# Kernel optimization log

Hardware: AMD Instinct MI355X
Metric: run time of the kernel (lower is better)

Reference implementation:

```python
import jax, jax.numpy as jnp
import numpy as np

B, N, I, H, O, E, HD = 4, 2048, 32, 64, 32, 2, 2  # batch, nodes, in_dim, hidden, out, edgetypes, heads
D1 = H * HD * E  # layer-1 filter input dim (concat of all heads/edgetypes from layer 0)


def setup_inputs() -> dict:
    key = jax.random.key(0)
    ks = jax.random.split(key, 20)
    s = 0.1
    return {
        "nodes": jax.random.normal(ks[0], (B, N, I), jnp.float32),
        "edges": jax.random.normal(ks[1], (B, N, N, E), jnp.float32),
        "W_emb": jax.random.normal(ks[2], (I, H), jnp.float32) * s,
        "b_emb": jnp.zeros((H,), jnp.float32),
        "Wf0": jax.random.normal(ks[3], (E, HD, H, H), jnp.float32) * s,
        "w1_0": jax.random.normal(ks[4], (E, HD, H), jnp.float32) * s,
        "b1_0": jnp.zeros((E, HD), jnp.float32),
        "w2_0": jax.random.normal(ks[5], (E, HD, H), jnp.float32) * s,
        "b2_0": jnp.zeros((E, HD), jnp.float32),
        "bias0": jax.random.normal(ks[6], (HD, H), jnp.float32) * s,  # state_bias aliased across edgetypes (list-mult bug)
        "Wf1": jax.random.normal(ks[7], (E, HD, D1, H), jnp.float32) * s,
        "w1_1": jax.random.normal(ks[8], (E, HD, H), jnp.float32) * s,
        "b1_1": jnp.zeros((E, HD), jnp.float32),
        "w2_1": jax.random.normal(ks[9], (E, HD, H), jnp.float32) * s,
        "b2_1": jnp.zeros((E, HD), jnp.float32),
        "bias1": jax.random.normal(ks[10], (HD, H), jnp.float32) * s,
        "W_out": jax.random.normal(ks[11], (H, O), jnp.float32) * s,
        "b_out": jnp.zeros((O,), jnp.float32),
    }


def _gat_layer(state, Wf, w1, b1, w2, b2, bias, edges_t, last):
    # state: (B,N,Din); Wf: (E,HD,Din,H); edges_t: (E,B,N,N)
    Wh = jnp.einsum('bnd,ehdk->ehbnk', state, Wf)                     # (E,HD,B,N,H)
    a1 = jnp.einsum('ehbnk,ehk->ehbn', Wh, w1) + b1[:, :, None, None]
    a2 = jnp.einsum('ehbnk,ehk->ehbn', Wh, w2) + b2[:, :, None, None]
    logits = jax.nn.leaky_relu(a1[..., :, None] + a2[..., None, :], 0.2) + edges_t[:, None]
    att = jax.nn.softmax(logits, axis=-2)                             # torch softmax dim=1 (over rows)
    msg = jnp.einsum('ehbik,ehbkd->ehbid', att, Wh) + bias[None, :, None, None, :]
    if last:
        return jnp.mean(jax.nn.elu(msg), axis=(0, 1))                 # (B,N,H)
    # concat in (edgetype-major, head-minor) order, matching the python loops
    return jnp.transpose(msg, (2, 3, 0, 1, 4)).reshape(msg.shape[2], msg.shape[3], -1)


def reference(nodes, edges, W_emb, b_emb, Wf0, w1_0, b1_0, w2_0, b2_0, bias0,
              Wf1, w1_1, b1_1, w2_1, b2_1, bias1, W_out, b_out):
    edges_t = jnp.transpose(edges, (3, 0, 1, 2))                      # (E,B,N,N)
    state = nodes @ W_emb + b_emb                                     # embedding
    state = _gat_layer(state, Wf0, w1_0, b1_0, w2_0, b2_0, bias0, edges_t, last=False)
    state = _gat_layer(state, Wf1, w1_1, b1_1, w2_1, b2_1, bias1, edges_t, last=True)
    out = state @ W_out + b_out                                       # (B,N,O)
    return jnp.mean(out, axis=1)                                      # graph-level output (B,O)
```

## Files before the change

kernel.cpp:

```cpp
#include <hip/hip_runtime.h>
#include <hip/hip_bf16.h>


constexpr int B_  = 4;
constexpr int N_  = 2048;
constexpr int I_  = 32;
constexpr int H_  = 64;
constexpr int O_  = 32;
constexpr int EH_ = 4;
constexpr int D1_ = 256;
constexpr int BN_ = B_ * N_;
constexpr int NC_ = 64;
constexpr int CH_ = N_ / NC_;
constexpr int TI_ = 16;
constexpr int TK_ = 32;
constexpr int NKT_ = N_ / TK_;
constexpr int NST_ = 32;

typedef __bf16 bf16x8 __attribute__((ext_vector_type(8)));
typedef float floatx4 __attribute__((ext_vector_type(4)));

constexpr float L2E_ = 1.4426950408889634f;

__device__ __forceinline__ unsigned short f2b(float f) {
    unsigned int u = __float_as_uint(f);
    return (unsigned short)((u + 0x7fffu + ((u >> 16) & 1u)) >> 16);
}

__device__ __forceinline__ float fexp2(float x) {
#if __has_builtin(__builtin_amdgcn_exp2f)
    return __builtin_amdgcn_exp2f(x);
#else
    return __expf(x * 0.6931471805599453f);
#endif
}

__device__ __forceinline__ void gl2lds16(const void* g, void* l) {
    __builtin_amdgcn_global_load_lds(
        (const __attribute__((address_space(1))) unsigned int*)g,
        (__attribute__((address_space(3))) unsigned int*)l, 16, 0, 0);
}

__global__ __launch_bounds__(256) void prep_kernel(
        const float* __restrict__ nodes, const float* __restrict__ W_emb,
        const float* __restrict__ b_emb, const float* __restrict__ Wf0,
        const float* __restrict__ Wf1, unsigned short* __restrict__ state0B,
        unsigned short* __restrict__ WfB0, unsigned short* __restrict__ WfB1) {
    int blk = blockIdx.x;
    int t = threadIdx.x;
    __shared__ float sn[4][I_];
    if (blk < 2048) {
        int r = t >> 6, h = t & 63;
        if (t < 4 * I_) {
            int rr = t / I_, ii = t % I_;
            sn[rr][ii] = nodes[(size_t)(blk * 4 + rr) * I_ + ii];
        }
        __syncthreads();
        float acc = b_emb[h];
        #pragma unroll
        for (int i = 0; i < I_; ++i) acc += sn[r][i] * W_emb[i * H_ + h];
        state0B[(size_t)(blk * 4 + r) * H_ + h] = f2b(acc);
    } else if (blk < 2048 + 64) {
        int o = (blk - 2048) * 256 + t;
        int k = o & 63, n = (o >> 6) & 63, c = o >> 12;
        WfB0[o] = f2b(Wf0[((size_t)c * 64 + k) * 64 + n]);
    } else {
        int o = (blk - 2112) * 256 + t;
        int k = o & 255, n = (o >> 8) & 63, c = o >> 14;
        WfB1[o] = f2b(Wf1[((size_t)c * 256 + k) * 64 + n]);
    }
}

template <int DIN>
__global__ __launch_bounds__(256) void wh_a_mfma_kernel(
        const unsigned short* __restrict__ stateB, const unsigned short* __restrict__ WfB,
        const float* __restrict__ w1, const float* __restrict__ b1,
        const float* __restrict__ w2, const float* __restrict__ b2,
        unsigned short* __restrict__ WhB, float* __restrict__ a1,
        float* __restrict__ a2) {
    int t = threadIdx.x;
    int lane = t & 63, wv = t >> 6;
    int col = lane & 15, qd = lane >> 4;
    int bn0 = blockIdx.x * TI_;
    int b = bn0 >> 11;

    floatx4 acc[4] = {{0,0,0,0},{0,0,0,0},{0,0,0,0},{0,0,0,0}};
    const unsigned short* __restrict__ ap = stateB + (size_t)(bn0 + col) * DIN + qd * 8;
    const unsigned short* __restrict__ bp = WfB + ((size_t)(wv * 64 + col) * DIN + qd * 8);
    #pragma unroll
    for (int k0 = 0; k0 < DIN; k0 += 32) {
        bf16x8 af = *(const bf16x8*)(ap + k0);
        #pragma unroll
        for (int nt = 0; nt < 4; ++nt) {
            bf16x8 bf = *(const bf16x8*)(bp + (size_t)nt * 16 * DIN + k0);
            acc[nt] = __builtin_amdgcn_mfma_f32_16x16x32_bf16(af, bf, acc[nt], 0, 0, 0);
        }
    }
    int nb = ((bn0 & 2047) >> 3) + (qd >> 1);
    #pragma unroll
    for (int nt = 0; nt < 4; ++nt) {
        unsigned int lo = (unsigned int)f2b(acc[nt][0]) | ((unsigned int)f2b(acc[nt][1]) << 16);
        unsigned int hi = (unsigned int)f2b(acc[nt][2]) | ((unsigned int)f2b(acc[nt][3]) << 16);
        uint2 v = make_uint2(lo, hi);
        *(uint2*)(WhB + ((((size_t)(wv * B_ + b) * 256 + nb) * 64 + nt * 16 + col) * 8
                         + (qd & 1) * 4)) = v;
    }
    float p1[4] = {}, p2[4] = {};
    #pragma unroll
    for (int nt = 0; nt < 4; ++nt) {
        float w1n = w1[wv * H_ + nt * 16 + col];
        float w2n = w2[wv * H_ + nt * 16 + col];
        #pragma unroll
        for (int r = 0; r < 4; ++r) {
            p1[r] += acc[nt][r] * w1n;
            p2[r] += acc[nt][r] * w2n;
        }
    }
    #pragma unroll
    for (int m = 1; m < 16; m <<= 1)
        #pragma unroll
        for (int r = 0; r < 4; ++r) {
            p1[r] += __shfl_xor(p1[r], m, 64);
            p2[r] += __shfl_xor(p2[r], m, 64);
        }
    if (col == 0) {
        float b1c = b1[wv], b2c = b2[wv];
        #pragma unroll
        for (int r = 0; r < 4; ++r) {
            a1[(size_t)wv * BN_ + bn0 + qd * 4 + r] = (p1[r] + b1c) * L2E_;
            a2[(size_t)wv * BN_ + bn0 + qd * 4 + r] = (p2[r] + b2c) * L2E_;
        }
    }
}

__global__ __launch_bounds__(256) void stats_kernel(
        const float* __restrict__ edges, const float* __restrict__ a1,
        const float* __restrict__ a2, float* __restrict__ ps) {
    int blk = blockIdx.x;
    int jt = blk & 3;
    int ic = (blk >> 2) & (NC_ - 1);
    int b  = blk >> 8;
    int t = threadIdx.x;
    int j0 = jt * 512 + t * 2;
    __shared__ float sa1[EH_][CH_];
    if (t < EH_ * CH_) {
        int cc = t >> 5, ii = t & 31;
        sa1[cc][ii] = a1[(size_t)cc * BN_ + b * N_ + ic * CH_ + ii];
    }
    __syncthreads();
    float a2x[EH_], a2y[EH_], s0[EH_], s1[EH_];
    #pragma unroll
    for (int cc = 0; cc < EH_; ++cc) {
        float2 av = *(const float2*)(a2 + (size_t)cc * BN_ + b * N_ + j0);
        a2x[cc] = av.x; a2y[cc] = av.y;
        s0[cc] = 0.f; s1[cc] = 0.f;
    }
    const float4* __restrict__ ep =
        (const float4*)edges + (((size_t)(b * N_ + ic * CH_) * N_ + j0) >> 1);
    #pragma unroll 4
    for (int ii = 0; ii < CH_; ++ii) {
        float4 u = ep[(size_t)ii * (N_ >> 1)];
        #pragma unroll
        for (int cc = 0; cc < EH_; ++cc) {
            float base = sa1[cc][ii];
            float xa = base + a2x[cc];
            float xb = base + a2y[cc];
            float la = fmaxf(xa, 0.2f * xa);
            float lb = fmaxf(xb, 0.2f * xb);
            float ea = (cc < 2) ? u.x : u.y;
            float eb = (cc < 2) ? u.z : u.w;
            s0[cc] += fexp2(fmaf(ea, L2E_, la));
            s1[cc] += fexp2(fmaf(eb, L2E_, lb));
        }
    }
    #pragma unroll
    for (int cc = 0; cc < EH_; ++cc)
        *(float2*)&ps[((size_t)ic * EH_ + cc) * BN_ + b * N_ + j0] =
            make_float2(s0[cc], s1[cc]);
}

__global__ __launch_bounds__(256) void scale_kernel(
        const float* __restrict__ ps, unsigned short* __restrict__ WhB) {
    int t = threadIdx.x;
    int m0 = blockIdx.x * 256;
    int cb = m0 >> 14;
    int c = cb >> 2, b = cb & 3;
    int k0 = ((m0 >> 6) & 255) * 8;
    __shared__ float sD[32];
    if (t < 32) {
        float S = 0.f;
        const float* pp = ps + (size_t)c * BN_ + b * N_ + k0 + t;
        #pragma unroll 8
        for (int ic = 0; ic < NC_; ++ic) S += pp[(size_t)ic * EH_ * BN_];
        sD[t] = 1.f / S;
    }
    __syncthreads();
    unsigned short* wp = WhB + (size_t)(m0 + t) * 8;
    uint4 w = *(const uint4*)wp;
    int nbo = (t >> 6) * 8;
    unsigned int words[4] = {w.x, w.y, w.z, w.w};
    #pragma unroll
    for (int q = 0; q < 4; ++q) {
        float lo = __uint_as_float((words[q] & 0xffffu) << 16) * sD[nbo + 2 * q];
        float hi = __uint_as_float(words[q] & 0xffff0000u) * sD[nbo + 2 * q + 1];
        words[q] = (unsigned)f2b(lo) | ((unsigned)f2b(hi) << 16);
    }
    *(uint4*)wp = make_uint4(words[0], words[1], words[2], words[3]);
}

template <int LAST>
__global__ __launch_bounds__(512, 4) void mac_kernel(
        const float* __restrict__ edges, const float* __restrict__ a1,
        const float* __restrict__ a2s, const unsigned short* __restrict__ WhB,
        const float* __restrict__ bias, void* __restrict__ outv) {
    int t = threadIdx.x;
    int blk0 = blockIdx.x;
    int blk = ((blk0 & 7) << 6) + (blk0 >> 3);
    int b = blk >> 7;
    int i0 = (blk & 127) * TI_;
    int lane = t & 63, wv = t >> 6;
    int c  = wv & 3;
    int kh = wv >> 2;
    int col = lane & 15;
    int qd  = lane >> 4;
    int esel = c >> 1;

    __shared__ float sa2[EH_][N_];
    __shared__ __attribute__((aligned(16))) unsigned char eds[3][2][TI_][256];
    __shared__ float sred[EH_][TI_][H_ + 1];

    for (int q = t; q < EH_ * (N_ / 4); q += 512) {
        int cc = q >> 9, kk = q & 511;
        ((float4*)sa2[cc])[kk] =
            ((const float4*)(a2s + (size_t)cc * BN_ + b * N_))[kk];
    }

    float a1v = a1[(size_t)c * BN_ + b * N_ + i0 + col];
    const unsigned short* __restrict__ whb0 = WhB + (size_t)(c * B_ + b) * (N_ * 64);

    int srow  = 4 * (wv & 3) + (lane >> 4);
    int sslot = (lane & 15) ^ (srow & 15);
    const char* gsrc = (const char*)edges
        + ((size_t)(b * N_ + i0 + srow) * N_ + (size_t)(wv >> 2) * 1024) * 8
        + sslot * 16;
    char* ldst = (char*)&eds[0][0][0][0] + wv * 1024;

    floatx4 acc[4] = {{0,0,0,0},{0,0,0,0},{0,0,0,0},{0,0,0,0}};

    gl2lds16(gsrc, ldst);
    for (int s = 0; s < NST_; ++s) {
        if (s + 1 < NST_)
            gl2lds16(gsrc + (size_t)(s + 1) * 256,
                     ldst + (size_t)(((s + 1) % 3)) * 8192);
        __syncthreads();

        int kt = kh * NST_ + s;
        const char* ebase = (const char*)&eds[0][0][0][0]
                          + (s % 3) * 8192 + kh * 4096 + col * 256;
        float ev[8];
        #pragma unroll
        for (int jj = 0; jj < 4; ++jj) {
            int sg = qd * 4 + jj;
            float4 v = *(const float4*)(ebase + ((sg ^ (col & 15)) * 16));
            ev[2 * jj]     = esel ? v.y : v.x;
            ev[2 * jj + 1] = esel ? v.w : v.z;
        }
        const float4* sp = (const float4*)&sa2[c][kt * TK_ + qd * 8];
        float4 z0 = sp[0], z1 = sp[1];
        float az[8] = {z0.x, z0.y, z0.z, z0.w, z1.x, z1.y, z1.z, z1.w};
        bf16x8 bf[4];
        #pragma unroll
        for (int nt = 0; nt < 4; ++nt)
            bf[nt] = *(const bf16x8*)(whb0 + ((size_t)(kt * 4 + qd) * 64 + nt * 16 + col) * 8);
        bf16x8 af;
        #pragma unroll
        for (int j = 0; j < 8; ++j) {
            float sx = a1v + az[j];
            float u  = fmaxf(sx, 0.2f * sx);
            af[j] = (__bf16)fexp2(fmaf(ev[j], L2E_, u));
        }
        #pragma unroll
        for (int nt = 0; nt < 4; ++nt)
            acc[nt] = __builtin_amdgcn_mfma_f32_16x16x32_bf16(af, bf[nt], acc[nt], 0, 0, 0);
    }

    if (kh == 1) {
        #pragma unroll
        for (int nt = 0; nt < 4; ++nt)
            #pragma unroll
            for (int r = 0; r < 4; ++r)
                sred[c][qd * 4 + r][nt * 16 + col] = acc[nt][r];
    }
    __syncthreads();
    if (kh == 0) {
        if (LAST) {
            #pragma unroll
            for (int nt = 0; nt < 4; ++nt) {
                float bb = bias[(c & 1) * H_ + nt * 16 + col];
                #pragma unroll
                for (int r = 0; r < 4; ++r) {
                    float x = acc[nt][r] + sred[c][qd * 4 + r][nt * 16 + col] + bb;
                    sred[c][qd * 4 + r][nt * 16 + col] =
                        x > 0.f ? x : (__expf(x) - 1.f);
                }
            }
        } else {
            unsigned short* out = (unsigned short*)outv;
            #pragma unroll
            for (int nt = 0; nt < 4; ++nt) {
                float bb = bias[(c & 1) * H_ + nt * 16 + col];
                #pragma unroll
                for (int r = 0; r < 4; ++r) {
                    float x = acc[nt][r] + sred[c][qd * 4 + r][nt * 16 + col] + bb;
                    out[((size_t)(b * N_ + i0 + qd * 4 + r)) * D1_ + c * H_ + nt * 16 + col]
                        = f2b(x);
                }
            }
        }
    }
    if (LAST) {
        __syncthreads();
        if (t < 64) {
            float s = 0.f;
            #pragma unroll
            for (int r = 0; r < TI_; ++r)
                s += sred[0][r][t] + sred[1][r][t] + sred[2][r][t] + sred[3][r][t];
            ((float*)outv)[(size_t)blk * 64 + t] = s * 0.25f;
        }
    }
}

__global__ __launch_bounds__(256) void out_kernel(
        const float* __restrict__ po, const float* __restrict__ W_out,
        const float* __restrict__ b_out, float* __restrict__ out) {
    int b = blockIdx.x, t = threadIdx.x;
    int d = t & 63, g0 = t >> 6;
    float s = 0.f;
    for (int g = g0; g < 128; g += 4) s += po[(size_t)(b * 128 + g) * 64 + d];
    __shared__ float red[4][H_];
    red[g0][d] = s;
    __syncthreads();
    if (t < H_) red[0][t] = (red[0][t] + red[1][t] + red[2][t] + red[3][t]) * (1.f / N_);
    __syncthreads();
    if (t < O_) {
        float acc = b_out[t];
        #pragma unroll 8
        for (int dd = 0; dd < H_; ++dd)
            acc += red[0][dd] * W_out[dd * O_ + t];
        out[b * O_ + t] = acc;
    }
}

extern "C" void kernel_launch(void* const* d_in, const int* in_sizes, int n_in,
                              void* d_out, int out_size, void* d_ws, size_t ws_size,
                              hipStream_t stream) {
    const float* nodes = (const float*)d_in[0];
    const float* edges = (const float*)d_in[1];
    const float* W_emb = (const float*)d_in[2];
    const float* b_emb = (const float*)d_in[3];
    const float* Wf0   = (const float*)d_in[4];
    const float* w1_0  = (const float*)d_in[5];
    const float* b1_0  = (const float*)d_in[6];
    const float* w2_0  = (const float*)d_in[7];
    const float* b2_0  = (const float*)d_in[8];
    const float* bias0 = (const float*)d_in[9];
    const float* Wf1   = (const float*)d_in[10];
    const float* w1_1  = (const float*)d_in[11];
    const float* b1_1  = (const float*)d_in[12];
    const float* w2_1  = (const float*)d_in[13];
    const float* b2_1  = (const float*)d_in[14];
    const float* bias1 = (const float*)d_in[15];
    const float* W_out = (const float*)d_in[16];
    const float* b_out = (const float*)d_in[17];

    float* ws = (float*)d_ws;
    unsigned short* state0B = (unsigned short*)ws;
    unsigned short* state1B = (unsigned short*)(ws + 262144);
    unsigned short* WhB  = (unsigned short*)(ws + 262144 + 1048576);
    unsigned short* WfB0 = (unsigned short*)(ws + 2359296);
    unsigned short* WfB1 = (unsigned short*)(ws + 2367488);
    float* a1 = ws + 2400256;
    float* a2 = ws + 2433024;
    float* ps = ws + 2465792;
    float* po = ws + 4562944;

    prep_kernel<<<2368, 256, 0, stream>>>(nodes, W_emb, b_emb, Wf0, Wf1,
                                          state0B, WfB0, WfB1);

    wh_a_mfma_kernel<H_><<<BN_ / TI_, 256, 0, stream>>>(state0B, WfB0, w1_0, b1_0,
                                                        w2_0, b2_0, WhB, a1, a2);
    stats_kernel<<<B_ * NC_ * (N_ / 512), 256, 0, stream>>>(edges, a1, a2, ps);
    scale_kernel<<<1024, 256, 0, stream>>>(ps, WhB);
    mac_kernel<0><<<B_ * (N_ / TI_), 512, 0, stream>>>(edges, a1, a2, WhB, bias0, state1B);
    wh_a_mfma_kernel<D1_><<<BN_ / TI_, 256, 0, stream>>>(state1B, WfB1, w1_1, b1_1,
                                                         w2_1, b2_1, WhB, a1, a2);
    stats_kernel<<<B_ * NC_ * (N_ / 512), 256, 0, stream>>>(edges, a1, a2, ps);
    scale_kernel<<<1024, 256, 0, stream>>>(ps, WhB);
    mac_kernel<1><<<B_ * (N_ / TI_), 512, 0, stream>>>(edges, a1, a2, WhB, bias1, po);

    out_kernel<<<B_, 256, 0, stream>>>(po, W_out, b_out, (float*)d_out);
}
```

Baseline: 372.8 us.

## Fuse softmax normalisation and output projection via atomic last-block reductions

```diff
diff --git a/kernel.cpp b/kernel.cpp
--- a/kernel.cpp
+++ b/kernel.cpp
@@ -11,10 +11,9 @@
 constexpr int D1_ = 256;
 constexpr int BN_ = B_ * N_;
 constexpr int NC_ = 64;
-constexpr int CH_ = N_ / NC_;
+constexpr int JT_ = 8;
 constexpr int TI_ = 16;
 constexpr int TK_ = 32;
-constexpr int NKT_ = N_ / TK_;
 constexpr int NST_ = 32;
 
 typedef __bf16 bf16x8 __attribute__((ext_vector_type(8)));
@@ -45,9 +44,17 @@
         const float* __restrict__ nodes, const float* __restrict__ W_emb,
         const float* __restrict__ b_emb, const float* __restrict__ Wf0,
         const float* __restrict__ Wf1, unsigned short* __restrict__ state0B,
-        unsigned short* __restrict__ WfB0, unsigned short* __restrict__ WfB1) {
+        unsigned short* __restrict__ WfB0, unsigned short* __restrict__ WfB1,
+        float* __restrict__ S, unsigned int* __restrict__ cnt,
+        float* __restrict__ acc, unsigned int* __restrict__ cnt2) {
     int blk = blockIdx.x;
     int t = threadIdx.x;
+    int gt = blk * 256 + t;
+    if (gt < EH_ * BN_) S[gt] = 0.f;
+    if (gt < B_ * JT_) cnt[gt] = 0u;
+    if (gt < B_ * H_) acc[gt] = 0.f;
+    if (gt < B_) cnt2[gt] = 0u;
+
     __shared__ float sn[4][I_];
     if (blk < 2048) {
         int r = t >> 6, h = t & 63;
@@ -56,10 +63,10 @@
             sn[rr][ii] = nodes[(size_t)(blk * 4 + rr) * I_ + ii];
         }
         __syncthreads();
-        float acc = b_emb[h];
-        #pragma unroll
-        for (int i = 0; i < I_; ++i) acc += sn[r][i] * W_emb[i * H_ + h];
-        state0B[(size_t)(blk * 4 + r) * H_ + h] = f2b(acc);
+        float a = b_emb[h];
+        #pragma unroll
+        for (int i = 0; i < I_; ++i) a += sn[r][i] * W_emb[i * H_ + h];
+        state0B[(size_t)(blk * 4 + r) * H_ + h] = f2b(a);
     } else if (blk < 2048 + 64) {
         int o = (blk - 2048) * 256 + t;
         int k = o & 63, n = (o >> 6) & 63, c = o >> 12;
@@ -135,84 +142,86 @@
 
 __global__ __launch_bounds__(256) void stats_kernel(
         const float* __restrict__ edges, const float* __restrict__ a1,
-        const float* __restrict__ a2, float* __restrict__ ps) {
+        const float* __restrict__ a2, float* __restrict__ S,
+        unsigned int* __restrict__ cnt, unsigned short* __restrict__ WhB) {
     int blk = blockIdx.x;
-    int jt = blk & 3;
-    int ic = (blk >> 2) & (NC_ - 1);
-    int b  = blk >> 8;
+    int jt = blk & 7;
+    int ic = (blk >> 3) & 63;
+    int b  = blk >> 9;
     int t = threadIdx.x;
-    int j0 = jt * 512 + t * 2;
-    __shared__ float sa1[EH_][CH_];
-    if (t < EH_ * CH_) {
+    int j = jt * 256 + t;
+    __shared__ float sa1[EH_][32];
+    __shared__ float sInv[EH_][256];
+    __shared__ unsigned int sflag;
+    if (t < 128) {
         int cc = t >> 5, ii = t & 31;
-        sa1[cc][ii] = a1[(size_t)cc * BN_ + b * N_ + ic * CH_ + ii];
+        sa1[cc][ii] = a1[(size_t)cc * BN_ + b * N_ + ic * 32 + ii];
     }
     __syncthreads();
-    float a2x[EH_], a2y[EH_], s0[EH_], s1[EH_];
+    float a2v[EH_], s[EH_];
     #pragma unroll
     for (int cc = 0; cc < EH_; ++cc) {
-        float2 av = *(const float2*)(a2 + (size_t)cc * BN_ + b * N_ + j0);
-        a2x[cc] = av.x; a2y[cc] = av.y;
-        s0[cc] = 0.f; s1[cc] = 0.f;
-    }
-    const float4* __restrict__ ep =
-        (const float4*)edges + (((size_t)(b * N_ + ic * CH_) * N_ + j0) >> 1);
+        a2v[cc] = a2[(size_t)cc * BN_ + b * N_ + j];
+        s[cc] = 0.f;
+    }
+    const float2* __restrict__ ep =
+        (const float2*)edges + (size_t)(b * N_ + ic * 32) * N_ + j;
     #pragma unroll 4
-    for (int ii = 0; ii < CH_; ++ii) {
-        float4 u = ep[(size_t)ii * (N_ >> 1)];
+    for (int ii = 0; ii < 32; ++ii) {
+        float2 u = ep[(size_t)ii * N_];
         #pragma unroll
         for (int cc = 0; cc < EH_; ++cc) {
-            float base = sa1[cc][ii];
-            float xa = base + a2x[cc];
-            float xb = base + a2y[cc];
-            float la = fmaxf(xa, 0.2f * xa);
-            float lb = fmaxf(xb, 0.2f * xb);
-            float ea = (cc < 2) ? u.x : u.y;
-            float eb = (cc < 2) ? u.z : u.w;
-            s0[cc] += fexp2(fmaf(ea, L2E_, la));
-            s1[cc] += fexp2(fmaf(eb, L2E_, lb));
+            float x = sa1[cc][ii] + a2v[cc];
+            float l = fmaxf(x, 0.2f * x);
+            s[cc] += fexp2(fmaf((cc < 2) ? u.x : u.y, L2E_, l));
         }
     }
     #pragma unroll
     for (int cc = 0; cc < EH_; ++cc)
-        *(float2*)&ps[((size_t)ic * EH_ + cc) * BN_ + b * N_ + j0] =
-            make_float2(s0[cc], s1[cc]);
-}
-
-__global__ __launch_bounds__(256) void scale_kernel(
-        const float* __restrict__ ps, unsigned short* __restrict__ WhB) {
-    int t = threadIdx.x;
-    int m0 = blockIdx.x * 256;
-    int cb = m0 >> 14;
-    int c = cb >> 2, b = cb & 3;
-    int k0 = ((m0 >> 6) & 255) * 8;
-    __shared__ float sD[32];
-    if (t < 32) {
-        float S = 0.f;
-        const float* pp = ps + (size_t)c * BN_ + b * N_ + k0 + t;
-        #pragma unroll 8
-        for (int ic = 0; ic < NC_; ++ic) S += pp[(size_t)ic * EH_ * BN_];
-        sD[t] = 1.f / S;
-    }
+        atomicAdd(&S[(size_t)cc * BN_ + b * N_ + j], s[cc]);
+    __threadfence();
     __syncthreads();
-    unsigned short* wp = WhB + (size_t)(m0 + t) * 8;
-    uint4 w = *(const uint4*)wp;
-    int nbo = (t >> 6) * 8;
-    unsigned int words[4] = {w.x, w.y, w.z, w.w};
-    #pragma unroll
-    for (int q = 0; q < 4; ++q) {
-        float lo = __uint_as_float((words[q] & 0xffffu) << 16) * sD[nbo + 2 * q];
-        float hi = __uint_as_float(words[q] & 0xffff0000u) * sD[nbo + 2 * q + 1];
-        words[q] = (unsigned)f2b(lo) | ((unsigned)f2b(hi) << 16);
-    }
-    *(uint4*)wp = make_uint4(words[0], words[1], words[2], words[3]);
+    if (t == 0) sflag = atomicAdd(&cnt[b * JT_ + jt], 1u);
+    __syncthreads();
+    if (sflag == NC_ - 1) {
+        __threadfence();
+        for (int q = t; q < EH_ * 256; q += 256) {
+            int cc = q >> 8, kk = q & 255;
+            float Sv = atomicAdd(&S[(size_t)cc * BN_ + b * N_ + jt * 256 + kk], 0.f);
+            sInv[cc][kk] = 1.f / Sv;
+        }
+        __syncthreads();
+        for (int q = t; q < 8192; q += 256) {
+            int cc  = q >> 11;
+            int nbl = (q >> 6) & 31;
+            int ncol = q & 63;
+            uint4* wp = (uint4*)WhB
+                + (((size_t)(cc * B_ + b) * 256 + jt * 32 + nbl) * 64 + ncol);
+            int k0 = nbl * 8;
+            uint4 w = *wp;
+            unsigned int words[4] = {w.x, w.y, w.z, w.w};
+            #pragma unroll
+            for (int qq = 0; qq < 4; ++qq) {
+                float lo = __uint_as_float((words[qq] & 0xffffu) << 16)
+                         * sInv[cc][k0 + 2 * qq];
+                float hi = __uint_as_float(words[qq] & 0xffff0000u)
+                         * sInv[cc][k0 + 2 * qq + 1];
+                words[qq] = (unsigned)f2b(lo) | ((unsigned)f2b(hi) << 16);
+            }
+            *wp = make_uint4(words[0], words[1], words[2], words[3]);
+        }
+    }
 }
 
 template <int LAST>
 __global__ __launch_bounds__(512, 4) void mac_kernel(
         const float* __restrict__ edges, const float* __restrict__ a1,
         const float* __restrict__ a2s, const unsigned short* __restrict__ WhB,
-        const float* __restrict__ bias, void* __restrict__ outv) {
+        const float* __restrict__ bias, void* __restrict__ outv,
+        float* __restrict__ Sz, unsigned int* __restrict__ cntz,
+        float* __restrict__ accg, unsigned int* __restrict__ cnt2,
+        const float* __restrict__ W_out, const float* __restrict__ b_out,
+        float* __restrict__ outF) {
     int t = threadIdx.x;
     int blk0 = blockIdx.x;
     int blk = ((blk0 & 7) << 6) + (blk0 >> 3);
@@ -225,9 +234,16 @@
     int qd  = lane >> 4;
     int esel = c >> 1;
 
+    if (!LAST) {
+        if (t < 64) Sz[(size_t)blk * 64 + t] = 0.f;
+        if (blk0 == 0 && t >= 64 && t < 64 + B_ * JT_) cntz[t - 64] = 0u;
+    }
+
     __shared__ float sa2[EH_][N_];
     __shared__ __attribute__((aligned(16))) unsigned char eds[3][2][TI_][256];
     __shared__ float sred[EH_][TI_][H_ + 1];
+    __shared__ unsigned int sflag;
+    __shared__ float sacc[H_];
 
     for (int q = t; q < EH_ * (N_ / 4); q += 512) {
         int cc = q >> 9, kk = q & 511;
@@ -249,19 +265,18 @@
 
     gl2lds16(gsrc, ldst);
     for (int s = 0; s < NST_; ++s) {
+        __syncthreads();
         if (s + 1 < NST_)
             gl2lds16(gsrc + (size_t)(s + 1) * 256,
                      ldst + (size_t)(((s + 1) % 3)) * 8192);
-        __syncthreads();
-
         int kt = kh * NST_ + s;
-        const char* ebase = (const char*)&eds[0][0][0][0]
+        const unsigned char* ebase = (const unsigned char*)&eds[0][0][0][0]
                           + (s % 3) * 8192 + kh * 4096 + col * 256;
         float ev[8];
         #pragma unroll
         for (int jj = 0; jj < 4; ++jj) {
             int sg = qd * 4 + jj;
-            float4 v = *(const float4*)(ebase + ((sg ^ (col & 15)) * 16));
+            float4 v = *(const float4*)(ebase + ((sg ^ col) * 16));
             ev[2 * jj]     = esel ? v.y : v.x;
             ev[2 * jj + 1] = esel ? v.w : v.z;
         }
@@ -274,10 +289,10 @@
             bf[nt] = *(const bf16x8*)(whb0 + ((size_t)(kt * 4 + qd) * 64 + nt * 16 + col) * 8);
         bf16x8 af;
         #pragma unroll
-        for (int j = 0; j < 8; ++j) {
-            float sx = a1v + az[j];
+        for (int jv = 0; jv < 8; ++jv) {
+            float sx = a1v + az[jv];
             float u  = fmaxf(sx, 0.2f * sx);
-            af[j] = (__bf16)fexp2(fmaf(ev[j], L2E_, u));
+            af[jv] = (__bf16)fexp2(fmaf(ev[jv], L2E_, u));
         }
         #pragma unroll
         for (int nt = 0; nt < 4; ++nt)
@@ -299,9 +314,9 @@
                 float bb = bias[(c & 1) * H_ + nt * 16 + col];
                 #pragma unroll
                 for (int r = 0; r < 4; ++r) {
-                    float x = acc[nt][r] + sred[c][qd * 4 + r][nt * 16 + col] + bb;
+                    float xv = acc[nt][r] + sred[c][qd * 4 + r][nt * 16 + col] + bb;
                     sred[c][qd * 4 + r][nt * 16 + col] =
-                        x > 0.f ? x : (__expf(x) - 1.f);
+                        xv > 0.f ? xv : (__expf(xv) - 1.f);
                 }
             }
         } else {
@@ -311,9 +326,9 @@
                 float bb = bias[(c & 1) * H_ + nt * 16 + col];
                 #pragma unroll
                 for (int r = 0; r < 4; ++r) {
-                    float x = acc[nt][r] + sred[c][qd * 4 + r][nt * 16 + col] + bb;
+                    float xv = acc[nt][r] + sred[c][qd * 4 + r][nt * 16 + col] + bb;
                     out[((size_t)(b * N_ + i0 + qd * 4 + r)) * D1_ + c * H_ + nt * 16 + col]
-                        = f2b(x);
+                        = f2b(xv);
                 }
             }
         }
@@ -325,29 +340,25 @@
             #pragma unroll
             for (int r = 0; r < TI_; ++r)
                 s += sred[0][r][t] + sred[1][r][t] + sred[2][r][t] + sred[3][r][t];
-            ((float*)outv)[(size_t)blk * 64 + t] = s * 0.25f;
-        }
-    }
-}
-
-__global__ __launch_bounds__(256) void out_kernel(
-        const float* __restrict__ po, const float* __restrict__ W_out,
-        const float* __restrict__ b_out, float* __restrict__ out) {
-    int b = blockIdx.x, t = threadIdx.x;
-    int d = t & 63, g0 = t >> 6;
-    float s = 0.f;
-    for (int g = g0; g < 128; g += 4) s += po[(size_t)(b * 128 + g) * 64 + d];
-    __shared__ float red[4][H_];
-    red[g0][d] = s;
-    __syncthreads();
-    if (t < H_) red[0][t] = (red[0][t] + red[1][t] + red[2][t] + red[3][t]) * (1.f / N_);
-    __syncthreads();
-    if (t < O_) {
-        float acc = b_out[t];
-        #pragma unroll 8
-        for (int dd = 0; dd < H_; ++dd)
-            acc += red[0][dd] * W_out[dd * O_ + t];
-        out[b * O_ + t] = acc;
+            atomicAdd(&accg[b * H_ + t], s * 0.25f);
+        }
+        __threadfence();
+        __syncthreads();
+        if (t == 0) sflag = atomicAdd(&cnt2[b], 1u);
+        __syncthreads();
+        if (sflag == 127) {
+            __threadfence();
+            if (t < H_)
+                sacc[t] = atomicAdd(&accg[b * H_ + t], 0.f) * (1.f / N_);
+            __syncthreads();
+            if (t < O_) {
+                float o = b_out[t];
+                #pragma unroll 8
+                for (int dd = 0; dd < H_; ++dd)
+                    o += sacc[dd] * W_out[dd * O_ + t];
+                outF[b * O_ + t] = o;
+            }
+        }
     }
 }
 
@@ -376,27 +387,29 @@
     float* ws = (float*)d_ws;
     unsigned short* state0B = (unsigned short*)ws;
     unsigned short* state1B = (unsigned short*)(ws + 262144);
-    unsigned short* WhB  = (unsigned short*)(ws + 262144 + 1048576);
+    unsigned short* WhB  = (unsigned short*)(ws + 1310720);
     unsigned short* WfB0 = (unsigned short*)(ws + 2359296);
     unsigned short* WfB1 = (unsigned short*)(ws + 2367488);
     float* a1 = ws + 2400256;
     float* a2 = ws + 2433024;
-    float* ps = ws + 2465792;
-    float* po = ws + 4562944;
+    float* S  = ws + 2465792;
+    unsigned int* cnt  = (unsigned int*)(ws + 2498560);
+    float* accg        = ws + 2498592;
+    unsigned int* cnt2 = (unsigned int*)(ws + 2498848);
 
     prep_kernel<<<2368, 256, 0, stream>>>(nodes, W_emb, b_emb, Wf0, Wf1,
-                                          state0B, WfB0, WfB1);
+                                          state0B, WfB0, WfB1, S, cnt, accg, cnt2);
 
     wh_a_mfma_kernel<H_><<<BN_ / TI_, 256, 0, stream>>>(state0B, WfB0, w1_0, b1_0,
                                                         w2_0, b2_0, WhB, a1, a2);
-    stats_kernel<<<B_ * NC_ * (N_ / 512), 256, 0, stream>>>(edges, a1, a2, ps);
-    scale_kernel<<<1024, 256, 0, stream>>>(ps, WhB);
-    mac_kernel<0><<<B_ * (N_ / TI_), 512, 0, stream>>>(edges, a1, a2, WhB, bias0, state1B);
+    stats_kernel<<<B_ * NC_ * JT_, 256, 0, stream>>>(edges, a1, a2, S, cnt, WhB);
+    mac_kernel<0><<<B_ * (N_ / TI_), 512, 0, stream>>>(
+        edges, a1, a2, WhB, bias0, state1B, S, cnt, accg, cnt2, W_out, b_out,
+        (float*)d_out);
     wh_a_mfma_kernel<D1_><<<BN_ / TI_, 256, 0, stream>>>(state1B, WfB1, w1_1, b1_1,
                                                          w2_1, b2_1, WhB, a1, a2);
-    stats_kernel<<<B_ * NC_ * (N_ / 512), 256, 0, stream>>>(edges, a1, a2, ps);
-    scale_kernel<<<1024, 256, 0, stream>>>(ps, WhB);
-    mac_kernel<1><<<B_ * (N_ / TI_), 512, 0, stream>>>(edges, a1, a2, WhB, bias1, po);
-
-    out_kernel<<<B_, 256, 0, stream>>>(po, W_out, b_out, (float*)d_out);
-}
+    stats_kernel<<<B_ * NC_ * JT_, 256, 0, stream>>>(edges, a1, a2, S, cnt, WhB);
+    mac_kernel<1><<<B_ * (N_ / TI_), 512, 0, stream>>>(
+        edges, a1, a2, WhB, bias1, state1B, S, cnt, accg, cnt2, W_out, b_out,
+        (float*)d_out);
+}
```

Result: slower. 957.5 us (+156.9%).
